# Kernel tuning notes

Measured on AMD Instinct MI355X. Metric: run time of the kernel, lower is better.

Reference implementation:

```python
import jax, jax.numpy as jnp
from jax import lax
import numpy as np

D, H, W3 = 240, 144, 240
V = D * H * W3  # 8294400 voxels


def conv3d(x, w, padding, stride=(1, 1, 1), b=None):
    y = lax.conv_general_dilated(x, w, window_strides=stride, padding=padding,
                                 dimension_numbers=('NCDHW', 'OIDHW', 'NCDHW'))
    if b is not None:
        y = y + b[None, :, None, None, None]
    return y


def downsample_block(x, w):
    # conv(c_in -> c_out - c_in, k3 s2 p1) concat maxpool(2,2), then relu
    c = conv3d(x, w, [(1, 1)] * 3, stride=(2, 2, 2))
    p = lax.reduce_window(x, -jnp.inf, lax.max, (1, 1, 2, 2, 2), (1, 1, 2, 2, 2), 'VALID')
    return jax.nn.relu(jnp.concatenate([c, p], axis=1))


def bottleneck(x, w_in, w133, b133, w331, b331, w313, b313, w_out):
    y0 = jax.nn.relu(conv3d(x, w_in, [(0, 0)] * 3))
    y1 = jax.nn.relu(conv3d(y0, w133, [(0, 0), (1, 1), (1, 1)], b=b133))
    y2 = jax.nn.relu(conv3d(y1, w331, [(1, 1), (1, 1), (0, 0)], b=b331) + y1)
    y3 = jax.nn.relu(conv3d(y2, w313, [(1, 1), (0, 0), (1, 1)], b=b313) + y2 + y1)
    return jax.nn.relu(conv3d(y3, w_out, [(0, 0)] * 3) + x)  # residual=True


def project2d_3d(feature2d, depth_3d):
    b, c, h, w = feature2d.shape
    flat = feature2d.reshape(b, c, h * w)

    def one(feat, depth):  # feat [c, HW], depth [HW]
        # pixels with depth<=0 are redirected out of bounds and dropped (stay zero)
        idx = jnp.where(depth > 0, depth, V)
        out = jnp.zeros((V, feat.shape[0]), feat.dtype).at[idx].set(feat.T, mode='drop')
        return out.T  # [c, V]

    return jax.vmap(one)(flat, depth_3d).reshape(b, c, D, H, W3)


def setup_inputs() -> dict:
    key = jax.random.key(0)
    ks = jax.random.split(key, 20)
    f = lambda i, shape: jax.random.normal(ks[i], shape, jnp.float32) * 0.05
    return {
        'feature2d': jax.random.normal(ks[0], (1, 12, 480, 640), jnp.float32),
        'depth_3d': jax.random.randint(ks[1], (1, 480 * 640), 0, V),
        'w_ds1': f(2, (4, 12, 3, 3, 3)),
        'b1_w_in': f(3, (4, 16, 1, 1, 1)),
        'b1_w133': f(4, (4, 4, 1, 3, 3)), 'b1_b133': f(5, (4,)),
        'b1_w331': f(6, (4, 4, 3, 3, 1)), 'b1_b331': f(7, (4,)),
        'b1_w313': f(8, (4, 4, 3, 1, 3)), 'b1_b313': f(9, (4,)),
        'b1_w_out': f(10, (16, 4, 1, 1, 1)),
        'w_ds2': f(11, (16, 16, 3, 3, 3)),
        'b2_w_in': f(12, (8, 32, 1, 1, 1)),
        'b2_w133': f(13, (8, 8, 1, 3, 3)), 'b2_b133': f(14, (8,)),
        'b2_w331': f(15, (8, 8, 3, 3, 1)), 'b2_b331': f(16, (8,)),
        'b2_w313': f(17, (8, 8, 3, 1, 3)), 'b2_b313': f(18, (8,)),
        'b2_w_out': f(19, (32, 8, 1, 1, 1)),
    }


def reference(feature2d, depth_3d, w_ds1,
              b1_w_in, b1_w133, b1_b133, b1_w331, b1_b331, b1_w313, b1_b313, b1_w_out,
              w_ds2,
              b2_w_in, b2_w133, b2_b133, b2_w331, b2_b331, b2_w313, b2_b313, b2_w_out):
    # location == 'late'
    segres = project2d_3d(feature2d, depth_3d)  # [b,12,240,144,240]
    # AvgPool3d(k=3, p=1, s=1) with count_include_pad=True -> window sum / 27
    pool = lax.reduce_window(segres, 0.0, lax.add, (1, 1, 3, 3, 3), (1, 1, 1, 1, 1),
                             [(0, 0), (0, 0), (1, 1), (1, 1), (1, 1)]) / 27.0
    segres = segres + pool * (segres == 0).astype(segres.dtype)
    x = downsample_block(segres, w_ds1)  # [b,16,120,72,120]
    x = bottleneck(x, b1_w_in, b1_w133, b1_b133, b1_w331, b1_b331, b1_w313, b1_b313, b1_w_out)
    x = downsample_block(x, w_ds2)  # [b,32,60,36,60]
    x = bottleneck(x, b2_w_in, b2_w133, b2_b133, b2_w331, b2_b331, b2_w313, b2_b313, b2_w_out)
    return x
```

## Files before the change

kernel.cpp:

```cpp
#include <hip/hip_runtime.h>
#include <hip/hip_bf16.h>

typedef __hip_bfloat16 bf16;
typedef unsigned short u16;

static __device__ __forceinline__ float lo16(unsigned u) { return __uint_as_float(u << 16); }
static __device__ __forceinline__ float hi16(unsigned u) { return __uint_as_float(u & 0xFFFF0000u); }
static __device__ __forceinline__ unsigned f2u(float x) {
    unsigned u = __float_as_uint(x);
    return (u + 0x7FFFu + ((u >> 16) & 1u)) >> 16;
}
static __device__ __forceinline__ unsigned pack2(float a, float b) {
    return f2u(a) | (f2u(b) << 16);
}

constexpr int D0 = 240, H0 = 144, W0 = 240;
constexpr int V  = D0 * H0 * W0;
constexpr int NPIX = 480 * 640;
constexpr int D1 = 120, H1 = 72, W1 = 120;
constexpr int N1 = D1 * H1 * W1;
constexpr int D2 = 60, H2 = 36, W2 = 60;
constexpr int N2 = D2 * H2 * W2;

constexpr size_t GRP_U16  = (size_t)V * 4;
constexpr size_t GRP_BYTES = GRP_U16 * sizeof(u16);
constexpr size_t SEG_BYTES = 3 * GRP_BYTES;
constexpr size_t WIN_BYTES = (size_t)V * sizeof(unsigned);
constexpr int ZCHUNKS  = (int)((SEG_BYTES + WIN_BYTES) / 16);
constexpr int WCHUNKS  = (int)(WIN_BYTES / 16);
constexpr size_t BIG_WS = SEG_BYTES + WIN_BYTES + GRP_BYTES;

__global__ void __launch_bounds__(256) kz_zero16(uint4* __restrict__ p, int nchunks) {
    int i = blockIdx.x * 256 + threadIdx.x;
    if (i >= nchunks) return;
    p[i] = make_uint4(0u, 0u, 0u, 0u);
}

__global__ void __launch_bounds__(256) kz_scatter_win(const int* __restrict__ depth,
                                                      unsigned* __restrict__ winner) {
    int p = blockIdx.x * 256 + threadIdx.x;
    if (p >= NPIX) return;
    int d = depth[p];
    if (d > 0 && d < V) atomicMax(&winner[d], (unsigned)(p + 1));
}

__global__ void __launch_bounds__(256) kz_scatter_write(const int* __restrict__ depth,
                                                        const unsigned* __restrict__ winner,
                                                        const float* __restrict__ feat,
                                                        u16* __restrict__ seg) {
    int p = blockIdx.x * 256 + threadIdx.x;
    if (p >= NPIX) return;
    int d = depth[p];
    if (d > 0 && d < V && winner[d] == (unsigned)(p + 1)) {
#pragma unroll
        for (int g = 0; g < 3; ++g) {
            uint2 val;
            val.x = pack2(feat[(4 * g + 0) * NPIX + p], feat[(4 * g + 1) * NPIX + p]);
            val.y = pack2(feat[(4 * g + 2) * NPIX + p], feat[(4 * g + 3) * NPIX + p]);
            *(uint2*)(seg + g * GRP_U16 + (size_t)d * 4) = val;
        }
    }
}

constexpr int FTW = 120;
constexpr int FROWS = 36;

template <bool GATED>
__global__ void __launch_bounds__(256) kz_fillL(const u16* __restrict__ rb,
                                                const unsigned* __restrict__ win,
                                                u16* __restrict__ fb) {
    __shared__ u16 S[FROWS * FTW * 4];
    int bid = blockIdx.x;
    int wt = bid & 1;
    int t1 = bid >> 1;
    int ht = t1 % 36;
    int dt = t1 / 36;
    int d0 = dt * 4, h0 = ht * 4, w0 = wt * 120;
    int tid = threadIdx.x;

    for (int tt = tid; tt < FROWS * 60; tt += 256) {
        int hr = tt / 60;
        int pt = tt - hr * 60;
        int w = w0 + 2 * pt;
        int d = d0 - 1 + hr / 6;
        int h = h0 - 1 + hr % 6;
        uint4 O = make_uint4(0u, 0u, 0u, 0u);
        if (d >= 0 && d < D0 && h >= 0 && h < H0) {
            size_t row = (size_t)(d * H0 + h) * W0;
            const u16* rp = rb + (row + w) * 4;
            uint4 X = *(const uint4*)(rp);
            if (GATED) {
                uint2 WN = *(const uint2*)(win + row + w);
                if (WN.x == 0u) { X.x = 0u; X.y = 0u; }
                if (WN.y == 0u) { X.z = 0u; X.w = 0u; }
            }
            float x0[4] = {lo16(X.x), hi16(X.x), lo16(X.y), hi16(X.y)};
            float x1[4] = {lo16(X.z), hi16(X.z), lo16(X.w), hi16(X.w)};
            float l[4] = {0.f, 0.f, 0.f, 0.f}, rr[4] = {0.f, 0.f, 0.f, 0.f};
            if (w > 0) {
                uint2 L = *(const uint2*)(rp - 4);
                if (GATED && win[row + w - 1] == 0u) { L.x = 0u; L.y = 0u; }
                l[0] = lo16(L.x); l[1] = hi16(L.x); l[2] = lo16(L.y); l[3] = hi16(L.y);
            }
            if (w < 238) {
                uint2 R = *(const uint2*)(rp + 8);
                if (GATED && win[row + w + 2] == 0u) { R.x = 0u; R.y = 0u; }
                rr[0] = lo16(R.x); rr[1] = hi16(R.x); rr[2] = lo16(R.y); rr[3] = hi16(R.y);
            }
            O.x = pack2(l[0] + x0[0] + x1[0], l[1] + x0[1] + x1[1]);
            O.y = pack2(l[2] + x0[2] + x1[2], l[3] + x0[3] + x1[3]);
            O.z = pack2(x0[0] + x1[0] + rr[0], x0[1] + x1[1] + rr[1]);
            O.w = pack2(x0[2] + x1[2] + rr[2], x0[3] + x1[3] + rr[3]);
        }
        *(uint4*)(S + ((size_t)hr * FTW + 2 * pt) * 4) = O;
    }
    __syncthreads();

    for (int ot = tid; ot < 16 * 60; ot += 256) {
        int orr = ot / 60;
        int pt = ot - orr * 60;
        int w = w0 + 2 * pt;
        int di = orr >> 2, hi_ = orr & 3;
        int d = d0 + di, h = h0 + hi_;
        float s[8] = {0.f, 0.f, 0.f, 0.f, 0.f, 0.f, 0.f, 0.f};
#pragma unroll
        for (int dd = 0; dd < 3; ++dd) {
#pragma unroll
            for (int dh = 0; dh < 3; ++dh) {
                int hr = (di + dd) * 6 + (hi_ + dh);
                uint4 T = *(const uint4*)(S + ((size_t)hr * FTW + 2 * pt) * 4);
                s[0] += lo16(T.x); s[1] += hi16(T.x); s[2] += lo16(T.y); s[3] += hi16(T.y);
                s[4] += lo16(T.z); s[5] += hi16(T.z); s[6] += lo16(T.w); s[7] += hi16(T.w);
            }
        }
        size_t row = (size_t)(d * H0 + h) * W0;
        size_t gi = (row + w) * 4;
        uint4 Rv = *(const uint4*)(rb + gi);
        if (GATED) {
            uint2 WN = *(const uint2*)(win + row + w);
            if (WN.x == 0u) { Rv.x = 0u; Rv.y = 0u; }
            if (WN.y == 0u) { Rv.z = 0u; Rv.w = 0u; }
        }
        constexpr float inv27 = 1.0f / 27.0f;
        uint4 Ov;
        Ov.x = ((Rv.x & 0x7FFFu) ? (Rv.x & 0xFFFFu) : f2u(s[0] * inv27))
             | ((((Rv.x >> 16) & 0x7FFFu) ? (Rv.x >> 16) : f2u(s[1] * inv27)) << 16);
        Ov.y = ((Rv.y & 0x7FFFu) ? (Rv.y & 0xFFFFu) : f2u(s[2] * inv27))
             | ((((Rv.y >> 16) & 0x7FFFu) ? (Rv.y >> 16) : f2u(s[3] * inv27)) << 16);
        Ov.z = ((Rv.z & 0x7FFFu) ? (Rv.z & 0xFFFFu) : f2u(s[4] * inv27))
             | ((((Rv.z >> 16) & 0x7FFFu) ? (Rv.z >> 16) : f2u(s[5] * inv27)) << 16);
        Ov.w = ((Rv.w & 0x7FFFu) ? (Rv.w & 0xFFFFu) : f2u(s[6] * inv27))
             | ((((Rv.w >> 16) & 0x7FFFu) ? (Rv.w >> 16) : f2u(s[7] * inv27)) << 16);
        *(uint4*)(fb + gi) = Ov;
    }
}

#define SEL2(ci, x0, x1) ((ci) == 0 ? lo16(x0) : (ci) == 1 ? hi16(x0) : (ci) == 2 ? lo16(x1) : hi16(x1))

template <bool FUSE_PW>
__global__ void __launch_bounds__(256) kz_ds1(const u16* __restrict__ f0g,
                                              const u16* __restrict__ f1g,
                                              const u16* __restrict__ f2g,
                                              const float* __restrict__ w,
                                              const float* __restrict__ wpw,
                                              float* __restrict__ x1i,
                                              float* __restrict__ y0o) {
    __shared__ float wl[12 * 27 * 4];
    __shared__ float wpl[64];
    for (int t = threadIdx.x; t < 12 * 27 * 4; t += 256) {
        int m = t & 3;
        int r = t >> 2;
        int tap = r % 27;
        int ci12 = r / 27;
        wl[t] = w[(m * 12 + ci12) * 27 + tap];
    }
    if (FUSE_PW && threadIdx.x < 64) wpl[threadIdx.x] = wpw[threadIdx.x];
    __syncthreads();
    int tq = blockIdx.x * 256 + threadIdx.x;
    if (tq >= N1 / 4) return;
    int q  = tq % 30;
    int t2 = tq / 30;
    int ho = t2 % H1;
    int d0 = t2 / H1;
    size_t o0 = (size_t)tq * 4;
    int vbase = 8 * q;

    const u16* bases[3] = {f0g, f1g, f2g};
    float acc[4][4];
    float mxp[3][4][4];
#pragma unroll
    for (int j = 0; j < 4; ++j)
#pragma unroll
        for (int m = 0; m < 4; ++m) acc[j][m] = 0.f;
#pragma unroll
    for (int g = 0; g < 3; ++g)
#pragma unroll
        for (int ci = 0; ci < 4; ++ci)
#pragma unroll
            for (int j = 0; j < 4; ++j) mxp[g][ci][j] = -1e30f;

#pragma unroll
    for (int g = 0; g < 3; ++g) {
        const u16* base = bases[g];
        const float* wg = wl + g * 432;
#pragma unroll 1
        for (int kd = 0; kd < 3; ++kd) {
            int d2 = 2 * d0 - 1 + kd;
            bool dv = (d2 >= 0 && d2 < D0);
#pragma unroll
            for (int kh = 0; kh < 3; ++kh) {
                int h2 = 2 * ho - 1 + kh;
                bool vv = dv && (h2 >= 0) && (h2 < H0);
                uint2 E = make_uint2(0u, 0u);
                uint4 A = make_uint4(0u, 0u, 0u, 0u);
                uint4 B = A, C = A, D = A;
                if (vv) {
                    const u16* rp = base + ((size_t)(d2 * H0 + h2) * W0 + vbase) * 4;
                    A = *(const uint4*)(rp);
                    B = *(const uint4*)(rp + 8);
                    C = *(const uint4*)(rp + 16);
                    D = *(const uint4*)(rp + 24);
                    if (q > 0) E = *(const uint2*)(rp - 4);
                }
                const float* wk = wg + (kd * 9 + kh * 3) * 4;
#pragma unroll
                for (int ci = 0; ci < 4; ++ci) {
                    float e  = SEL2(ci, E.x, E.y);
                    float a0 = SEL2(ci, A.x, A.y), a1 = SEL2(ci, A.z, A.w);
                    float b0 = SEL2(ci, B.x, B.y), b1 = SEL2(ci, B.z, B.w);
                    float c0 = SEL2(ci, C.x, C.y), c1 = SEL2(ci, C.z, C.w);
                    float e0 = SEL2(ci, D.x, D.y), e1 = SEL2(ci, D.z, D.w);
                    const float* wp_ = wk + ci * 108;
                    float4 wA = *(const float4*)(wp_);
                    float4 wB = *(const float4*)(wp_ + 4);
                    float4 wC = *(const float4*)(wp_ + 8);
                    acc[0][0] += e  * wA.x + a0 * wB.x + a1 * wC.x;
                    acc[0][1] += e  * wA.y + a0 * wB.y + a1 * wC.y;
                    acc[0][2] += e  * wA.z + a0 * wB.z + a1 * wC.z;
                    acc[0][3] += e  * wA.w + a0 * wB.w + a1 * wC.w;
                    acc[1][0] += a1 * wA.x + b0 * wB.x + b1 * wC.x;
                    acc[1][1] += a1 * wA.y + b0 * wB.y + b1 * wC.y;
                    acc[1][2] += a1 * wA.z + b0 * wB.z + b1 * wC.z;
                    acc[1][3] += a1 * wA.w + b0 * wB.w + b1 * wC.w;
                    acc[2][0] += b1 * wA.x + c0 * wB.x + c1 * wC.x;
                    acc[2][1] += b1 * wA.y + c0 * wB.y + c1 * wC.y;
                    acc[2][2] += b1 * wA.z + c0 * wB.z + c1 * wC.z;
                    acc[2][3] += b1 * wA.w + c0 * wB.w + c1 * wC.w;
                    acc[3][0] += c1 * wA.x + e0 * wB.x + e1 * wC.x;
                    acc[3][1] += c1 * wA.y + e0 * wB.y + e1 * wC.y;
                    acc[3][2] += c1 * wA.z + e0 * wB.z + e1 * wC.z;
                    acc[3][3] += c1 * wA.w + e0 * wB.w + e1 * wC.w;
                    if (kh >= 1 && kd >= 1) {
                        mxp[g][ci][0] = fmaxf(mxp[g][ci][0], fmaxf(a0, a1));
                        mxp[g][ci][1] = fmaxf(mxp[g][ci][1], fmaxf(b0, b1));
                        mxp[g][ci][2] = fmaxf(mxp[g][ci][2], fmaxf(c0, c1));
                        mxp[g][ci][3] = fmaxf(mxp[g][ci][3], fmaxf(e0, e1));
                    }
                }
            }
        }
    }
#pragma unroll
    for (int j = 0; j < 4; ++j) {
        float x1v[16];
        x1v[0] = fmaxf(acc[j][0], 0.f); x1v[1] = fmaxf(acc[j][1], 0.f);
        x1v[2] = fmaxf(acc[j][2], 0.f); x1v[3] = fmaxf(acc[j][3], 0.f);
#pragma unroll
        for (int g = 0; g < 3; ++g) {
            x1v[4 + 4 * g + 0] = fmaxf(mxp[g][0][j], 0.f);
            x1v[4 + 4 * g + 1] = fmaxf(mxp[g][1][j], 0.f);
            x1v[4 + 4 * g + 2] = fmaxf(mxp[g][2][j], 0.f);
            x1v[4 + 4 * g + 3] = fmaxf(mxp[g][3][j], 0.f);
        }
        float* xo = x1i + (o0 + j) * 16;
        *(float4*)(xo)      = make_float4(x1v[0], x1v[1], x1v[2], x1v[3]);
        *(float4*)(xo + 4)  = make_float4(x1v[4], x1v[5], x1v[6], x1v[7]);
        *(float4*)(xo + 8)  = make_float4(x1v[8], x1v[9], x1v[10], x1v[11]);
        *(float4*)(xo + 12) = make_float4(x1v[12], x1v[13], x1v[14], x1v[15]);
        if (FUSE_PW) {
            float y[4];
#pragma unroll
            for (int m = 0; m < 4; ++m) {
                const float* wm = wpl + m * 16;
                float r = 0.f;
#pragma unroll
                for (int k = 0; k < 16; ++k) r += x1v[k] * wm[k];
                y[m] = fmaxf(r, 0.f);
            }
            *(float4*)(y0o + (o0 + j) * 4) = make_float4(y[0], y[1], y[2], y[3]);
        }
    }
}

__global__ void __launch_bounds__(256) kz_pw16to4i(const float* __restrict__ in,
                                                   const float* __restrict__ w,
                                                   float* __restrict__ out) {
    __shared__ float wl[64];
    if (threadIdx.x < 64) wl[threadIdx.x] = w[threadIdx.x];
    __syncthreads();
    int o = blockIdx.x * 256 + threadIdx.x;
    const float* ip = in + (size_t)o * 16;
    float4 A = *(const float4*)(ip);
    float4 B = *(const float4*)(ip + 4);
    float4 C = *(const float4*)(ip + 8);
    float4 D = *(const float4*)(ip + 12);
    float r[4];
#pragma unroll
    for (int m = 0; m < 4; ++m) {
        const float* wm = wl + m * 16;
        r[m] = A.x * wm[0] + A.y * wm[1] + A.z * wm[2] + A.w * wm[3]
             + B.x * wm[4] + B.y * wm[5] + B.z * wm[6] + B.w * wm[7]
             + C.x * wm[8] + C.y * wm[9] + C.z * wm[10] + C.w * wm[11]
             + D.x * wm[12] + D.y * wm[13] + D.z * wm[14] + D.w * wm[15];
    }
    *(float4*)(out + (size_t)o * 4) = make_float4(fmaxf(r[0], 0.f), fmaxf(r[1], 0.f),
                                                  fmaxf(r[2], 0.f), fmaxf(r[3], 0.f));
}

template <int KD, int KH, int KW, int NADD>
__global__ void __launch_bounds__(256) kz_bconv4i(const float* __restrict__ in,
                                                  const float* __restrict__ w,
                                                  const float* __restrict__ b,
                                                  const float* __restrict__ add1,
                                                  const float* __restrict__ add2,
                                                  float* __restrict__ out) {
    constexpr int S = KD * KH * KW;
    __shared__ float wl[16 * S];
    __shared__ float bl[4];
    for (int t = threadIdx.x; t < 16 * S; t += 256) {
        int m = t & 3;
        int r = t >> 2;
        int ci = r & 3;
        int tap = r >> 2;
        wl[t] = w[(m * 4 + ci) * S + tap];
    }
    if (threadIdx.x < 4) bl[threadIdx.x] = b[threadIdx.x];
    __syncthreads();
    int o = blockIdx.x * 256 + threadIdx.x;
    int wo = o % W1;
    int t  = o / W1;
    int ho = t % H1;
    int d0 = t / H1;
    float a0 = bl[0], a1 = bl[1], a2 = bl[2], a3 = bl[3];
#pragma unroll
    for (int kd = 0; kd < KD; ++kd) {
        int d2 = d0 + kd - KD / 2;
        if (KD > 1 && (d2 < 0 || d2 >= D1)) continue;
#pragma unroll
        for (int kh = 0; kh < KH; ++kh) {
            int h2 = ho + kh - KH / 2;
            if (KH > 1 && (h2 < 0 || h2 >= H1)) continue;
#pragma unroll
            for (int kw = 0; kw < KW; ++kw) {
                int w2 = wo + kw - KW / 2;
                if (KW > 1 && (w2 < 0 || w2 >= W1)) continue;
                float4 v = *(const float4*)(in + (size_t)((d2 * H1 + h2) * W1 + w2) * 4);
                int tap = (kd * KH + kh) * KW + kw;
                const float* wt = wl + tap * 16;
                float4 w0 = *(const float4*)(wt);
                float4 w1 = *(const float4*)(wt + 4);
                float4 w2v = *(const float4*)(wt + 8);
                float4 w3 = *(const float4*)(wt + 12);
                a0 += v.x * w0.x + v.y * w1.x + v.z * w2v.x + v.w * w3.x;
                a1 += v.x * w0.y + v.y * w1.y + v.z * w2v.y + v.w * w3.y;
                a2 += v.x * w0.z + v.y * w1.z + v.z * w2v.z + v.w * w3.z;
                a3 += v.x * w0.w + v.y * w1.w + v.z * w2v.w + v.w * w3.w;
            }
        }
    }
    if (NADD >= 1) {
        float4 r1 = *(const float4*)(add1 + (size_t)o * 4);
        a0 += r1.x; a1 += r1.y; a2 += r1.z; a3 += r1.w;
    }
    if (NADD >= 2) {
        float4 r2 = *(const float4*)(add2 + (size_t)o * 4);
        a0 += r2.x; a1 += r2.y; a2 += r2.z; a3 += r2.w;
    }
    *(float4*)(out + (size_t)o * 4) = make_float4(fmaxf(a0, 0.f), fmaxf(a1, 0.f),
                                                  fmaxf(a2, 0.f), fmaxf(a3, 0.f));
}

__global__ void __launch_bounds__(256) kz_bconv4i_pw(const float* __restrict__ in,
                                                     const float* __restrict__ w,
                                                     const float* __restrict__ b,
                                                     const float* __restrict__ add1,
                                                     const float* __restrict__ add2,
                                                     const float* __restrict__ wp,
                                                     const float* __restrict__ x1i,
                                                     float* __restrict__ out) {
    constexpr int S = 9;
    __shared__ float wl[16 * S];
    __shared__ float bl[4];
    __shared__ float wpl[64];
    for (int t = threadIdx.x; t < 16 * S; t += 256) {
        int m = t & 3;
        int r = t >> 2;
        int ci = r & 3;
        int tap = r >> 2;
        wl[t] = w[(m * 4 + ci) * S + tap];
    }
    if (threadIdx.x < 4) bl[threadIdx.x] = b[threadIdx.x];
    if (threadIdx.x < 64) wpl[threadIdx.x] = wp[threadIdx.x];
    __syncthreads();
    int o = blockIdx.x * 256 + threadIdx.x;
    int wo = o % W1;
    int t  = o / W1;
    int ho = t % H1;
    int d0 = t / H1;
    float a0 = bl[0], a1 = bl[1], a2 = bl[2], a3 = bl[3];
#pragma unroll
    for (int kd = 0; kd < 3; ++kd) {
        int d2 = d0 + kd - 1;
        if (d2 < 0 || d2 >= D1) continue;
#pragma unroll
        for (int kw = 0; kw < 3; ++kw) {
            int w2 = wo + kw - 1;
            if (w2 < 0 || w2 >= W1) continue;
            float4 v = *(const float4*)(in + (size_t)((d2 * H1 + ho) * W1 + w2) * 4);
            int tap = kd * 3 + kw;
            const float* wt = wl + tap * 16;
            float4 w0 = *(const float4*)(wt);
            float4 w1 = *(const float4*)(wt + 4);
            float4 w2v = *(const float4*)(wt + 8);
            float4 w3 = *(const float4*)(wt + 12);
            a0 += v.x * w0.x + v.y * w1.x + v.z * w2v.x + v.w * w3.x;
            a1 += v.x * w0.y + v.y * w1.y + v.z * w2v.y + v.w * w3.y;
            a2 += v.x * w0.z + v.y * w1.z + v.z * w2v.z + v.w * w3.z;
            a3 += v.x * w0.w + v.y * w1.w + v.z * w2v.w + v.w * w3.w;
        }
    }
    float4 r1 = *(const float4*)(add1 + (size_t)o * 4);
    float4 r2 = *(const float4*)(add2 + (size_t)o * 4);
    float y0 = fmaxf(a0 + r1.x + r2.x, 0.f);
    float y1 = fmaxf(a1 + r1.y + r2.y, 0.f);
    float y2 = fmaxf(a2 + r1.z + r2.z, 0.f);
    float y3 = fmaxf(a3 + r1.w + r2.w, 0.f);
    const float* rp = x1i + (size_t)o * 16;
    float4 R0 = *(const float4*)(rp);
    float4 R1 = *(const float4*)(rp + 4);
    float4 R2 = *(const float4*)(rp + 8);
    float4 R3 = *(const float4*)(rp + 12);
    float rr[16] = {R0.x, R0.y, R0.z, R0.w, R1.x, R1.y, R1.z, R1.w,
                    R2.x, R2.y, R2.z, R2.w, R3.x, R3.y, R3.z, R3.w};
#pragma unroll
    for (int m = 0; m < 16; ++m) {
        const float* wm = wpl + m * 4;
        float r = y0 * wm[0] + y1 * wm[1] + y2 * wm[2] + y3 * wm[3] + rr[m];
        out[(size_t)m * N1 + o] = fmaxf(r, 0.f);
    }
}

__global__ void __launch_bounds__(256) kz_ds2f(const float* __restrict__ in,
                                               const float* __restrict__ w,
                                               const float* __restrict__ wz,
                                               float* __restrict__ out,
                                               float* __restrict__ z0i) {
    __shared__ float wl[16 * 27 * 16];
    __shared__ float wzl[256];
    for (int t = threadIdx.x; t < 16 * 27 * 16; t += 256) {
        int m = t & 15;
        int r = t >> 4;
        int tap = r % 27;
        int ci = r / 27;
        wl[t] = w[(m * 16 + ci) * 27 + tap];
    }
    if (threadIdx.x < 256) {
        int m = threadIdx.x & 7;
        int k = threadIdx.x >> 3;
        wzl[threadIdx.x] = wz[m * 32 + k];
    }
    __syncthreads();
    int o = blockIdx.x * 256 + threadIdx.x;
    if (o >= N2) return;
    int wo = o % W2;
    int t  = o / W2;
    int ho = t % H2;
    int d0 = t / H2;
    float acc[16];
    float zacc[8];
#pragma unroll
    for (int m = 0; m < 16; ++m) acc[m] = 0.f;
#pragma unroll
    for (int m = 0; m < 8; ++m) zacc[m] = 0.f;
#pragma unroll 1
    for (int ci = 0; ci < 16; ++ci) {
        const float* base = in + ci * N1;
        const float* wci = wl + ci * 432;
        float mx = -1e30f;
#pragma unroll 1
        for (int kd = 0; kd < 3; ++kd) {
            int d2 = 2 * d0 - 1 + kd;
            bool dv = (d2 >= 0 && d2 < D1);
#pragma unroll
            for (int kh = 0; kh < 3; ++kh) {
                int h2 = 2 * ho - 1 + kh;
                bool rvv = dv && (h2 >= 0 && h2 < H1);
                float vm1 = 0.f, v0 = 0.f, v1 = 0.f;
                if (rvv) {
                    int r2 = (d2 * H1 + h2) * W1 + 2 * wo;
                    float2 pb = *(const float2*)(base + r2);
                    v0 = pb.x; v1 = pb.y;
                    if (wo > 0) {
                        float2 pa = *(const float2*)(base + r2 - 2);
                        vm1 = pa.y;
                    }
                }
                const float* wk = wci + (kd * 9 + kh * 3) * 16;
#pragma unroll
                for (int q = 0; q < 4; ++q) {
                    float4 wA = *(const float4*)(wk + q * 4);
                    float4 wB = *(const float4*)(wk + 16 + q * 4);
                    float4 wC = *(const float4*)(wk + 32 + q * 4);
                    acc[4 * q + 0] += vm1 * wA.x + v0 * wB.x + v1 * wC.x;
                    acc[4 * q + 1] += vm1 * wA.y + v0 * wB.y + v1 * wC.y;
                    acc[4 * q + 2] += vm1 * wA.z + v0 * wB.z + v1 * wC.z;
                    acc[4 * q + 3] += vm1 * wA.w + v0 * wB.w + v1 * wC.w;
                }
                if (kd >= 1 && kh >= 1) mx = fmaxf(mx, fmaxf(v0, v1));
            }
        }
        float pl = fmaxf(mx, 0.f);
        out[(16 + ci) * N2 + o] = pl;
        {
            const float* wq = wzl + (16 + ci) * 8;
            float4 z0 = *(const float4*)(wq);
            float4 z1 = *(const float4*)(wq + 4);
            zacc[0] += z0.x * pl; zacc[1] += z0.y * pl; zacc[2] += z0.z * pl; zacc[3] += z0.w * pl;
            zacc[4] += z1.x * pl; zacc[5] += z1.y * pl; zacc[6] += z1.z * pl; zacc[7] += z1.w * pl;
        }
    }
#pragma unroll
    for (int j = 0; j < 16; ++j) {
        float cj = fmaxf(acc[j], 0.f);
        out[j * N2 + o] = cj;
        const float* wq = wzl + j * 8;
        float4 z0 = *(const float4*)(wq);
        float4 z1 = *(const float4*)(wq + 4);
        zacc[0] += z0.x * cj; zacc[1] += z0.y * cj; zacc[2] += z0.z * cj; zacc[3] += z0.w * cj;
        zacc[4] += z1.x * cj; zacc[5] += z1.y * cj; zacc[6] += z1.z * cj; zacc[7] += z1.w * cj;
    }
    float* op = z0i + (size_t)o * 8;
    *(float4*)(op)     = make_float4(fmaxf(zacc[0], 0.f), fmaxf(zacc[1], 0.f),
                                     fmaxf(zacc[2], 0.f), fmaxf(zacc[3], 0.f));
    *(float4*)(op + 4) = make_float4(fmaxf(zacc[4], 0.f), fmaxf(zacc[5], 0.f),
                                     fmaxf(zacc[6], 0.f), fmaxf(zacc[7], 0.f));
}

template <int KD, int KH, int KW, int NADD>
__global__ void __launch_bounds__(256) kz_bconv8i(const float* __restrict__ in,
                                                  const float* __restrict__ w,
                                                  const float* __restrict__ b,
                                                  const float* __restrict__ add1,
                                                  const float* __restrict__ add2,
                                                  float* __restrict__ out) {
    constexpr int S = KD * KH * KW;
    __shared__ float wl[64 * S];
    __shared__ float bl[8];
    for (int t = threadIdx.x; t < 64 * S; t += 256) {
        int m = t & 7;
        int r = t >> 3;
        int ci = r & 7;
        int tap = r >> 3;
        wl[t] = w[(m * 8 + ci) * S + tap];
    }
    if (threadIdx.x < 8) bl[threadIdx.x] = b[threadIdx.x];
    __syncthreads();
    int o = blockIdx.x * 256 + threadIdx.x;
    if (o >= N2) return;
    int wo = o % W2;
    int t  = o / W2;
    int ho = t % H2;
    int d0 = t / H2;
    float acc[8];
#pragma unroll
    for (int m = 0; m < 8; ++m) acc[m] = bl[m];
#pragma unroll
    for (int kd = 0; kd < KD; ++kd) {
        int d2 = d0 + kd - KD / 2;
        if (KD > 1 && (d2 < 0 || d2 >= D2)) continue;
#pragma unroll
        for (int kh = 0; kh < KH; ++kh) {
            int h2 = ho + kh - KH / 2;
            if (KH > 1 && (h2 < 0 || h2 >= H2)) continue;
#pragma unroll
            for (int kw = 0; kw < KW; ++kw) {
                int w2 = wo + kw - KW / 2;
                if (KW > 1 && (w2 < 0 || w2 >= W2)) continue;
                const float* vp = in + (size_t)((d2 * H2 + h2) * W2 + w2) * 8;
                float4 v0 = *(const float4*)(vp);
                float4 v1 = *(const float4*)(vp + 4);
                float vv[8] = {v0.x, v0.y, v0.z, v0.w, v1.x, v1.y, v1.z, v1.w};
                int tap = (kd * KH + kh) * KW + kw;
                const float* wt = wl + tap * 64;
#pragma unroll
                for (int ci = 0; ci < 8; ++ci) {
                    float vc = vv[ci];
                    float4 wa = *(const float4*)(wt + ci * 8);
                    float4 wb = *(const float4*)(wt + ci * 8 + 4);
                    acc[0] += vc * wa.x; acc[1] += vc * wa.y;
                    acc[2] += vc * wa.z; acc[3] += vc * wa.w;
                    acc[4] += vc * wb.x; acc[5] += vc * wb.y;
                    acc[6] += vc * wb.z; acc[7] += vc * wb.w;
                }
            }
        }
    }
    if (NADD >= 1) {
        const float* ap = add1 + (size_t)o * 8;
        float4 r0 = *(const float4*)(ap), r1 = *(const float4*)(ap + 4);
        acc[0] += r0.x; acc[1] += r0.y; acc[2] += r0.z; acc[3] += r0.w;
        acc[4] += r1.x; acc[5] += r1.y; acc[6] += r1.z; acc[7] += r1.w;
    }
    if (NADD >= 2) {
        const float* ap = add2 + (size_t)o * 8;
        float4 r0 = *(const float4*)(ap), r1 = *(const float4*)(ap + 4);
        acc[0] += r0.x; acc[1] += r0.y; acc[2] += r0.z; acc[3] += r0.w;
        acc[4] += r1.x; acc[5] += r1.y; acc[6] += r1.z; acc[7] += r1.w;
    }
    float* op = out + (size_t)o * 8;
    *(float4*)(op)     = make_float4(fmaxf(acc[0], 0.f), fmaxf(acc[1], 0.f),
                                     fmaxf(acc[2], 0.f), fmaxf(acc[3], 0.f));
    *(float4*)(op + 4) = make_float4(fmaxf(acc[4], 0.f), fmaxf(acc[5], 0.f),
                                     fmaxf(acc[6], 0.f), fmaxf(acc[7], 0.f));
}

__global__ void __launch_bounds__(256) kz_bconv8i_pw(const float* __restrict__ in,
                                                     const float* __restrict__ w,
                                                     const float* __restrict__ b,
                                                     const float* __restrict__ add1,
                                                     const float* __restrict__ add2,
                                                     const float* __restrict__ wp,
                                                     const float* __restrict__ resp,
                                                     float* __restrict__ out) {
    constexpr int S = 9;
    __shared__ float wl[64 * S];
    __shared__ float bl[8];
    __shared__ float wpl[256];
    for (int t = threadIdx.x; t < 64 * S; t += 256) {
        int m = t & 7;
        int r = t >> 3;
        int ci = r & 7;
        int tap = r >> 3;
        wl[t] = w[(m * 8 + ci) * S + tap];
    }
    if (threadIdx.x < 8) bl[threadIdx.x] = b[threadIdx.x];
    if (threadIdx.x < 256) wpl[threadIdx.x] = wp[threadIdx.x];
    __syncthreads();
    int o = blockIdx.x * 256 + threadIdx.x;
    if (o >= N2) return;
    int wo = o % W2;
    int t  = o / W2;
    int ho = t % H2;
    int d0 = t / H2;
    float acc[8];
#pragma unroll
    for (int m = 0; m < 8; ++m) acc[m] = bl[m];
#pragma unroll
    for (int kd = 0; kd < 3; ++kd) {
        int d2 = d0 + kd - 1;
        if (d2 < 0 || d2 >= D2) continue;
#pragma unroll
        for (int kw = 0; kw < 3; ++kw) {
            int w2 = wo + kw - 1;
            if (w2 < 0 || w2 >= W2) continue;
            const float* vp = in + (size_t)((d2 * H2 + ho) * W2 + w2) * 8;
            float4 v0 = *(const float4*)(vp);
            float4 v1 = *(const float4*)(vp + 4);
            float vv[8] = {v0.x, v0.y, v0.z, v0.w, v1.x, v1.y, v1.z, v1.w};
            int tap = kd * 3 + kw;
            const float* wt = wl + tap * 64;
#pragma unroll
            for (int ci = 0; ci < 8; ++ci) {
                float vc = vv[ci];
                float4 wa = *(const float4*)(wt + ci * 8);
                float4 wb = *(const float4*)(wt + ci * 8 + 4);
                acc[0] += vc * wa.x; acc[1] += vc * wa.y;
                acc[2] += vc * wa.z; acc[3] += vc * wa.w;
                acc[4] += vc * wb.x; acc[5] += vc * wb.y;
                acc[6] += vc * wb.z; acc[7] += vc * wb.w;
            }
        }
    }
    {
        const float* ap = add1 + (size_t)o * 8;
        float4 r0 = *(const float4*)(ap), r1 = *(const float4*)(ap + 4);
        acc[0] += r0.x; acc[1] += r0.y; acc[2] += r0.z; acc[3] += r0.w;
        acc[4] += r1.x; acc[5] += r1.y; acc[6] += r1.z; acc[7] += r1.w;
    }
    {
        const float* ap = add2 + (size_t)o * 8;
        float4 r0 = *(const float4*)(ap), r1 = *(const float4*)(ap + 4);
        acc[0] += r0.x; acc[1] += r0.y; acc[2] += r0.z; acc[3] += r0.w;
        acc[4] += r1.x; acc[5] += r1.y; acc[6] += r1.z; acc[7] += r1.w;
    }
#pragma unroll
    for (int m = 0; m < 8; ++m) acc[m] = fmaxf(acc[m], 0.f);
#pragma unroll
    for (int m = 0; m < 32; ++m) {
        const float* wm = wpl + m * 8;
        float r = acc[0] * wm[0] + acc[1] * wm[1] + acc[2] * wm[2] + acc[3] * wm[3]
                + acc[4] * wm[4] + acc[5] * wm[5] + acc[6] * wm[6] + acc[7] * wm[7];
        r += resp[(size_t)m * N2 + o];
        out[(size_t)m * N2 + o] = fmaxf(r, 0.f);
    }
}

extern "C" void kernel_launch(void* const* d_in, const int* in_sizes, int n_in,
                              void* d_out, int out_size, void* d_ws, size_t ws_size,
                              hipStream_t stream) {
    const float* feat   = (const float*)d_in[0];
    const int*   depth  = (const int*)d_in[1];
    const float* w_ds1  = (const float*)d_in[2];
    const float* b1_win = (const float*)d_in[3];
    const float* b1w133 = (const float*)d_in[4];
    const float* b1b133 = (const float*)d_in[5];
    const float* b1w331 = (const float*)d_in[6];
    const float* b1b331 = (const float*)d_in[7];
    const float* b1w313 = (const float*)d_in[8];
    const float* b1b313 = (const float*)d_in[9];
    const float* b1wout = (const float*)d_in[10];
    const float* w_ds2  = (const float*)d_in[11];
    const float* b2_win = (const float*)d_in[12];
    const float* b2w133 = (const float*)d_in[13];
    const float* b2b133 = (const float*)d_in[14];
    const float* b2w331 = (const float*)d_in[15];
    const float* b2b331 = (const float*)d_in[16];
    const float* b2w313 = (const float*)d_in[17];
    const float* b2b313 = (const float*)d_in[18];
    const float* b2wout = (const float*)d_in[19];

    char* base = (char*)d_ws;
    const bool bigws = (ws_size >= BIG_WS);

    u16* raw0 = (u16*)base;
    u16* raw1 = (u16*)(base + GRP_BYTES);
    u16* raw2 = (u16*)(base + 2 * GRP_BYTES);
    unsigned* winner = (unsigned*)(base + SEG_BYTES);
    u16* fil0 = bigws ? (u16*)(base + SEG_BYTES + WIN_BYTES) : (u16*)(base + SEG_BYTES);
    u16* fil1 = (u16*)base;
    u16* fil2 = (u16*)(base + GRP_BYTES);
    float* x1i = (float*)(base + 2 * GRP_BYTES);
    float* y0i = bigws ? (float*)(base + SEG_BYTES) : (float*)base;
    float* y1i = bigws ? (float*)base : (float*)base + 4 * N1;
    float* y2i = y1i + 4 * N1;
    float* x1b = (float*)(base + SEG_BYTES);
    float* x2  = (float*)base;
    float* z0i = x2 + 32 * N2;
    float* z1i = z0i + 8 * N2;
    float* z2i = z1i + 8 * N2;

    float* out = (float*)d_out;

    if (bigws) {
        kz_zero16<<<WCHUNKS / 256, 256, 0, stream>>>((uint4*)winner, WCHUNKS);
    } else {
        kz_zero16<<<ZCHUNKS / 256, 256, 0, stream>>>((uint4*)base, ZCHUNKS);
    }

    kz_scatter_win  <<<NPIX / 256, 256, 0, stream>>>(depth, winner);
    kz_scatter_write<<<NPIX / 256, 256, 0, stream>>>(depth, winner, feat, raw0);

    if (bigws) {
        kz_fillL<true><<<4320, 256, 0, stream>>>(raw0, winner, fil0);
        kz_fillL<true><<<4320, 256, 0, stream>>>(raw1, winner, fil1);
        kz_fillL<true><<<4320, 256, 0, stream>>>(raw2, winner, fil2);
    } else {
        kz_fillL<false><<<4320, 256, 0, stream>>>(raw0, nullptr, fil0);
        kz_fillL<false><<<4320, 256, 0, stream>>>(raw1, nullptr, fil1);
        kz_fillL<false><<<4320, 256, 0, stream>>>(raw2, nullptr, fil2);
    }

    if (bigws) {
        kz_ds1<true><<<(N1 / 4 + 255) / 256, 256, 0, stream>>>(fil0, fil1, fil2, w_ds1,
                                                               b1_win, x1i, y0i);
    } else {
        kz_ds1<false><<<(N1 / 4 + 255) / 256, 256, 0, stream>>>(fil0, fil1, fil2, w_ds1,
                                                                nullptr, x1i, nullptr);
        kz_pw16to4i<<<N1 / 256, 256, 0, stream>>>(x1i, b1_win, y0i);
    }

    kz_bconv4i<1, 3, 3, 0><<<N1 / 256, 256, 0, stream>>>(y0i, b1w133, b1b133, nullptr, nullptr, y1i);
    kz_bconv4i<3, 3, 1, 1><<<N1 / 256, 256, 0, stream>>>(y1i, b1w331, b1b331, y1i, nullptr, y2i);
    kz_bconv4i_pw<<<N1 / 256, 256, 0, stream>>>(y2i, b1w313, b1b313, y2i, y1i, b1wout, x1i, x1b);

    kz_ds2f<<<(N2 + 255) / 256, 256, 0, stream>>>(x1b, w_ds2, b2_win, x2, z0i);

    kz_bconv8i<1, 3, 3, 0><<<(N2 + 255) / 256, 256, 0, stream>>>(z0i, b2w133, b2b133, nullptr, nullptr, z1i);
    kz_bconv8i<3, 3, 1, 1><<<(N2 + 255) / 256, 256, 0, stream>>>(z1i, b2w331, b2b331, z1i, nullptr, z2i);
    kz_bconv8i_pw<<<(N2 + 255) / 256, 256, 0, stream>>>(z2i, b2w313, b2b313, z2i, z1i, b2wout, x2, out);

    (void)in_sizes; (void)n_in; (void)out_size;
}
```

Measured before the change: 649.0 us.

## Register-block bottleneck convs and ds2 over consecutive W outputs

The stage-1 bottleneck conv kernels now have each thread compute four consecutive W outputs, loading a six-voxel row strip once and reusing it across the three kw taps. The final pointwise step writes float4 vectors. The stage-2 downsample kernel computes two adjacent outputs per thread, sharing overlapping input loads and writing float2. This cuts redundant global loads and index arithmetic, at the cost of more registers per thread and fewer threads in flight.

```diff
diff --git a/kernel.cpp b/kernel.cpp
--- a/kernel.cpp
+++ b/kernel.cpp
@@ -318,7 +318,7 @@
 }
 
 template <int KD, int KH, int KW, int NADD>
-__global__ void __launch_bounds__(256) kz_bconv4i(const float* __restrict__ in,
+__global__ void __launch_bounds__(256) kz_bconv4p(const float* __restrict__ in,
                                                   const float* __restrict__ w,
                                                   const float* __restrict__ b,
                                                   const float* __restrict__ add1,
@@ -336,12 +336,18 @@
     }
     if (threadIdx.x < 4) bl[threadIdx.x] = b[threadIdx.x];
     __syncthreads();
-    int o = blockIdx.x * 256 + threadIdx.x;
-    int wo = o % W1;
-    int t  = o / W1;
-    int ho = t % H1;
-    int d0 = t / H1;
-    float a0 = bl[0], a1 = bl[1], a2 = bl[2], a3 = bl[3];
+    int tq = blockIdx.x * 256 + threadIdx.x;
+    if (tq >= N1 / 4) return;
+    int q  = tq % 30;
+    int t2 = tq / 30;
+    int ho = t2 % H1;
+    int d0 = t2 / H1;
+    size_t o0 = (size_t)tq * 4;
+    float acc[4][4];
+#pragma unroll
+    for (int j = 0; j < 4; ++j) {
+        acc[j][0] = bl[0]; acc[j][1] = bl[1]; acc[j][2] = bl[2]; acc[j][3] = bl[3];
+    }
 #pragma unroll
     for (int kd = 0; kd < KD; ++kd) {
         int d2 = d0 + kd - KD / 2;
@@ -350,37 +356,78 @@
         for (int kh = 0; kh < KH; ++kh) {
             int h2 = ho + kh - KH / 2;
             if (KH > 1 && (h2 < 0 || h2 >= H1)) continue;
-#pragma unroll
-            for (int kw = 0; kw < KW; ++kw) {
-                int w2 = wo + kw - KW / 2;
-                if (KW > 1 && (w2 < 0 || w2 >= W1)) continue;
-                float4 v = *(const float4*)(in + (size_t)((d2 * H1 + h2) * W1 + w2) * 4);
-                int tap = (kd * KH + kh) * KW + kw;
+            const float* rowp = in + (size_t)((d2 * H1 + h2) * W1 + 4 * q) * 4;
+            if (KW == 3) {
+                float4 vv[6];
+                vv[1] = *(const float4*)(rowp);
+                vv[2] = *(const float4*)(rowp + 4);
+                vv[3] = *(const float4*)(rowp + 8);
+                vv[4] = *(const float4*)(rowp + 12);
+                vv[0] = (q > 0)  ? *(const float4*)(rowp - 4)  : make_float4(0.f, 0.f, 0.f, 0.f);
+                vv[5] = (q < 29) ? *(const float4*)(rowp + 16) : make_float4(0.f, 0.f, 0.f, 0.f);
+#pragma unroll
+                for (int kw = 0; kw < 3; ++kw) {
+                    int tap = (kd * KH + kh) * 3 + kw;
+                    const float* wt = wl + tap * 16;
+                    float4 w0 = *(const float4*)(wt);
+                    float4 w1 = *(const float4*)(wt + 4);
+                    float4 w2v = *(const float4*)(wt + 8);
+                    float4 w3 = *(const float4*)(wt + 12);
+#pragma unroll
+                    for (int j = 0; j < 4; ++j) {
+                        float4 v = vv[j + kw];
+                        acc[j][0] += v.x * w0.x + v.y * w1.x + v.z * w2v.x + v.w * w3.x;
+                        acc[j][1] += v.x * w0.y + v.y * w1.y + v.z * w2v.y + v.w * w3.y;
+                        acc[j][2] += v.x * w0.z + v.y * w1.z + v.z * w2v.z + v.w * w3.z;
+                        acc[j][3] += v.x * w0.w + v.y * w1.w + v.z * w2v.w + v.w * w3.w;
+                    }
+                }
+            } else {
+                float4 vv[4];
+                vv[0] = *(const float4*)(rowp);
+                vv[1] = *(const float4*)(rowp + 4);
+                vv[2] = *(const float4*)(rowp + 8);
+                vv[3] = *(const float4*)(rowp + 12);
+                int tap = kd * KH + kh;
                 const float* wt = wl + tap * 16;
                 float4 w0 = *(const float4*)(wt);
                 float4 w1 = *(const float4*)(wt + 4);
                 float4 w2v = *(const float4*)(wt + 8);
                 float4 w3 = *(const float4*)(wt + 12);
-                a0 += v.x * w0.x + v.y * w1.x + v.z * w2v.x + v.w * w3.x;
-                a1 += v.x * w0.y + v.y * w1.y + v.z * w2v.y + v.w * w3.y;
-                a2 += v.x * w0.z + v.y * w1.z + v.z * w2v.z + v.w * w3.z;
-                a3 += v.x * w0.w + v.y * w1.w + v.z * w2v.w + v.w * w3.w;
+#pragma unroll
+                for (int j = 0; j < 4; ++j) {
+                    float4 v = vv[j];
+                    acc[j][0] += v.x * w0.x + v.y * w1.x + v.z * w2v.x + v.w * w3.x;
+                    acc[j][1] += v.x * w0.y + v.y * w1.y + v.z * w2v.y + v.w * w3.y;
+                    acc[j][2] += v.x * w0.z + v.y * w1.z + v.z * w2v.z + v.w * w3.z;
+                    acc[j][3] += v.x * w0.w + v.y * w1.w + v.z * w2v.w + v.w * w3.w;
+                }
             }
         }
     }
     if (NADD >= 1) {
-        float4 r1 = *(const float4*)(add1 + (size_t)o * 4);
-        a0 += r1.x; a1 += r1.y; a2 += r1.z; a3 += r1.w;
+#pragma unroll
+        for (int j = 0; j < 4; ++j) {
+            float4 r1 = *(const float4*)(add1 + (o0 + j) * 4);
+            acc[j][0] += r1.x; acc[j][1] += r1.y; acc[j][2] += r1.z; acc[j][3] += r1.w;
+        }
     }
     if (NADD >= 2) {
-        float4 r2 = *(const float4*)(add2 + (size_t)o * 4);
-        a0 += r2.x; a1 += r2.y; a2 += r2.z; a3 += r2.w;
-    }
-    *(float4*)(out + (size_t)o * 4) = make_float4(fmaxf(a0, 0.f), fmaxf(a1, 0.f),
-                                                  fmaxf(a2, 0.f), fmaxf(a3, 0.f));
-}
-
-__global__ void __launch_bounds__(256) kz_bconv4i_pw(const float* __restrict__ in,
+#pragma unroll
+        for (int j = 0; j < 4; ++j) {
+            float4 r2 = *(const float4*)(add2 + (o0 + j) * 4);
+            acc[j][0] += r2.x; acc[j][1] += r2.y; acc[j][2] += r2.z; acc[j][3] += r2.w;
+        }
+    }
+#pragma unroll
+    for (int j = 0; j < 4; ++j) {
+        *(float4*)(out + (o0 + j) * 4) =
+            make_float4(fmaxf(acc[j][0], 0.f), fmaxf(acc[j][1], 0.f),
+                        fmaxf(acc[j][2], 0.f), fmaxf(acc[j][3], 0.f));
+    }
+}
+
+__global__ void __launch_bounds__(256) kz_bconv4p_pw(const float* __restrict__ in,
                                                      const float* __restrict__ w,
                                                      const float* __restrict__ b,
                                                      const float* __restrict__ add1,
@@ -402,59 +449,88 @@
     if (threadIdx.x < 4) bl[threadIdx.x] = b[threadIdx.x];
     if (threadIdx.x < 64) wpl[threadIdx.x] = wp[threadIdx.x];
     __syncthreads();
-    int o = blockIdx.x * 256 + threadIdx.x;
-    int wo = o % W1;
-    int t  = o / W1;
-    int ho = t % H1;
-    int d0 = t / H1;
-    float a0 = bl[0], a1 = bl[1], a2 = bl[2], a3 = bl[3];
+    int tq = blockIdx.x * 256 + threadIdx.x;
+    if (tq >= N1 / 4) return;
+    int q  = tq % 30;
+    int t2 = tq / 30;
+    int ho = t2 % H1;
+    int d0 = t2 / H1;
+    size_t o0 = (size_t)tq * 4;
+    float acc[4][4];
+#pragma unroll
+    for (int j = 0; j < 4; ++j) {
+        acc[j][0] = bl[0]; acc[j][1] = bl[1]; acc[j][2] = bl[2]; acc[j][3] = bl[3];
+    }
 #pragma unroll
     for (int kd = 0; kd < 3; ++kd) {
         int d2 = d0 + kd - 1;
         if (d2 < 0 || d2 >= D1) continue;
+        const float* rowp = in + (size_t)((d2 * H1 + ho) * W1 + 4 * q) * 4;
+        float4 vv[6];
+        vv[1] = *(const float4*)(rowp);
+        vv[2] = *(const float4*)(rowp + 4);
+        vv[3] = *(const float4*)(rowp + 8);
+        vv[4] = *(const float4*)(rowp + 12);
+        vv[0] = (q > 0)  ? *(const float4*)(rowp - 4)  : make_float4(0.f, 0.f, 0.f, 0.f);
+        vv[5] = (q < 29) ? *(const float4*)(rowp + 16) : make_float4(0.f, 0.f, 0.f, 0.f);
 #pragma unroll
         for (int kw = 0; kw < 3; ++kw) {
-            int w2 = wo + kw - 1;
-            if (w2 < 0 || w2 >= W1) continue;
-            float4 v = *(const float4*)(in + (size_t)((d2 * H1 + ho) * W1 + w2) * 4);
             int tap = kd * 3 + kw;
             const float* wt = wl + tap * 16;
             float4 w0 = *(const float4*)(wt);
             float4 w1 = *(const float4*)(wt + 4);
             float4 w2v = *(const float4*)(wt + 8);
             float4 w3 = *(const float4*)(wt + 12);
-            a0 += v.x * w0.x + v.y * w1.x + v.z * w2v.x + v.w * w3.x;
-            a1 += v.x * w0.y + v.y * w1.y + v.z * w2v.y + v.w * w3.y;
-            a2 += v.x * w0.z + v.y * w1.z + v.z * w2v.z + v.w * w3.z;
-            a3 += v.x * w0.w + v.y * w1.w + v.z * w2v.w + v.w * w3.w;
-        }
-    }
-    float4 r1 = *(const float4*)(add1 + (size_t)o * 4);
-    float4 r2 = *(const float4*)(add2 + (size_t)o * 4);
-    float y0 = fmaxf(a0 + r1.x + r2.x, 0.f);
-    float y1 = fmaxf(a1 + r1.y + r2.y, 0.f);
-    float y2 = fmaxf(a2 + r1.z + r2.z, 0.f);
-    float y3 = fmaxf(a3 + r1.w + r2.w, 0.f);
-    const float* rp = x1i + (size_t)o * 16;
-    float4 R0 = *(const float4*)(rp);
-    float4 R1 = *(const float4*)(rp + 4);
-    float4 R2 = *(const float4*)(rp + 8);
-    float4 R3 = *(const float4*)(rp + 12);
-    float rr[16] = {R0.x, R0.y, R0.z, R0.w, R1.x, R1.y, R1.z, R1.w,
-                    R2.x, R2.y, R2.z, R2.w, R3.x, R3.y, R3.z, R3.w};
+#pragma unroll
+            for (int j = 0; j < 4; ++j) {
+                float4 v = vv[j + kw];
+                acc[j][0] += v.x * w0.x + v.y * w1.x + v.z * w2v.x + v.w * w3.x;
+                acc[j][1] += v.x * w0.y + v.y * w1.y + v.z * w2v.y + v.w * w3.y;
+                acc[j][2] += v.x * w0.z + v.y * w1.z + v.z * w2v.z + v.w * w3.z;
+                acc[j][3] += v.x * w0.w + v.y * w1.w + v.z * w2v.w + v.w * w3.w;
+            }
+        }
+    }
+    float y[4][4];
+#pragma unroll
+    for (int j = 0; j < 4; ++j) {
+        float4 r1 = *(const float4*)(add1 + (o0 + j) * 4);
+        float4 r2 = *(const float4*)(add2 + (o0 + j) * 4);
+        y[j][0] = fmaxf(acc[j][0] + r1.x + r2.x, 0.f);
+        y[j][1] = fmaxf(acc[j][1] + r1.y + r2.y, 0.f);
+        y[j][2] = fmaxf(acc[j][2] + r1.z + r2.z, 0.f);
+        y[j][3] = fmaxf(acc[j][3] + r1.w + r2.w, 0.f);
+    }
+    float rr[4][16];
+#pragma unroll
+    for (int j = 0; j < 4; ++j) {
+        const float* rp = x1i + (o0 + j) * 16;
+        float4 R0 = *(const float4*)(rp);
+        float4 R1 = *(const float4*)(rp + 4);
+        float4 R2 = *(const float4*)(rp + 8);
+        float4 R3 = *(const float4*)(rp + 12);
+        rr[j][0] = R0.x; rr[j][1] = R0.y; rr[j][2] = R0.z; rr[j][3] = R0.w;
+        rr[j][4] = R1.x; rr[j][5] = R1.y; rr[j][6] = R1.z; rr[j][7] = R1.w;
+        rr[j][8] = R2.x; rr[j][9] = R2.y; rr[j][10] = R2.z; rr[j][11] = R2.w;
+        rr[j][12] = R3.x; rr[j][13] = R3.y; rr[j][14] = R3.z; rr[j][15] = R3.w;
+    }
 #pragma unroll
     for (int m = 0; m < 16; ++m) {
         const float* wm = wpl + m * 4;
-        float r = y0 * wm[0] + y1 * wm[1] + y2 * wm[2] + y3 * wm[3] + rr[m];
-        out[(size_t)m * N1 + o] = fmaxf(r, 0.f);
-    }
-}
-
-__global__ void __launch_bounds__(256) kz_ds2f(const float* __restrict__ in,
-                                               const float* __restrict__ w,
-                                               const float* __restrict__ wz,
-                                               float* __restrict__ out,
-                                               float* __restrict__ z0i) {
+        float4 ov;
+        ov.x = fmaxf(y[0][0] * wm[0] + y[0][1] * wm[1] + y[0][2] * wm[2] + y[0][3] * wm[3] + rr[0][m], 0.f);
+        ov.y = fmaxf(y[1][0] * wm[0] + y[1][1] * wm[1] + y[1][2] * wm[2] + y[1][3] * wm[3] + rr[1][m], 0.f);
+        ov.z = fmaxf(y[2][0] * wm[0] + y[2][1] * wm[1] + y[2][2] * wm[2] + y[2][3] * wm[3] + rr[2][m], 0.f);
+        ov.w = fmaxf(y[3][0] * wm[0] + y[3][1] * wm[1] + y[3][2] * wm[2] + y[3][3] * wm[3] + rr[3][m], 0.f);
+        *(float4*)(out + (size_t)m * N1 + o0) = ov;
+    }
+}
+
+__global__ void __launch_bounds__(256) kz_ds2fp(const float* __restrict__ in,
+                                                const float* __restrict__ w,
+                                                const float* __restrict__ wz,
+                                                float* __restrict__ out,
+                                                float* __restrict__ z0i) {
     __shared__ float wl[16 * 27 * 16];
     __shared__ float wzl[256];
     for (int t = threadIdx.x; t < 16 * 27 * 16; t += 256) {
@@ -470,23 +546,27 @@
         wzl[threadIdx.x] = wz[m * 32 + k];
     }
     __syncthreads();
-    int o = blockIdx.x * 256 + threadIdx.x;
-    if (o >= N2) return;
-    int wo = o % W2;
-    int t  = o / W2;
-    int ho = t % H2;
-    int d0 = t / H2;
-    float acc[16];
-    float zacc[8];
-#pragma unroll
-    for (int m = 0; m < 16; ++m) acc[m] = 0.f;
-#pragma unroll
-    for (int m = 0; m < 8; ++m) zacc[m] = 0.f;
+    int tp = blockIdx.x * 256 + threadIdx.x;
+    if (tp >= N2 / 2) return;
+    int q  = tp % 30;
+    int t2 = tp / 30;
+    int ho = t2 % H2;
+    int d0 = t2 / H2;
+    size_t o0 = (size_t)tp * 2;
+    float acc[2][16];
+    float zacc[2][8];
+#pragma unroll
+    for (int j = 0; j < 2; ++j) {
+#pragma unroll
+        for (int m = 0; m < 16; ++m) acc[j][m] = 0.f;
+#pragma unroll
+        for (int m = 0; m < 8; ++m) zacc[j][m] = 0.f;
+    }
 #pragma unroll 1
     for (int ci = 0; ci < 16; ++ci) {
         const float* base = in + ci * N1;
         const float* wci = wl + ci * 432;
-        float mx = -1e30f;
+        float mx0 = -1e30f, mx1 = -1e30f;
 #pragma unroll 1
         for (int kd = 0; kd < 3; ++kd) {
             int d2 = 2 * d0 - 1 + kd;
@@ -495,55 +575,70 @@
             for (int kh = 0; kh < 3; ++kh) {
                 int h2 = 2 * ho - 1 + kh;
                 bool rvv = dv && (h2 >= 0 && h2 < H1);
-                float vm1 = 0.f, v0 = 0.f, v1 = 0.f;
+                float vin[5] = {0.f, 0.f, 0.f, 0.f, 0.f};
                 if (rvv) {
-                    int r2 = (d2 * H1 + h2) * W1 + 2 * wo;
-                    float2 pb = *(const float2*)(base + r2);
-                    v0 = pb.x; v1 = pb.y;
-                    if (wo > 0) {
+                    int r2 = (d2 * H1 + h2) * W1 + 4 * q;
+                    float4 pb = *(const float4*)(base + r2);
+                    vin[1] = pb.x; vin[2] = pb.y; vin[3] = pb.z; vin[4] = pb.w;
+                    if (q > 0) {
                         float2 pa = *(const float2*)(base + r2 - 2);
-                        vm1 = pa.y;
+                        vin[0] = pa.y;
                     }
                 }
                 const float* wk = wci + (kd * 9 + kh * 3) * 16;
 #pragma unroll
-                for (int q = 0; q < 4; ++q) {
-                    float4 wA = *(const float4*)(wk + q * 4);
-                    float4 wB = *(const float4*)(wk + 16 + q * 4);
-                    float4 wC = *(const float4*)(wk + 32 + q * 4);
-                    acc[4 * q + 0] += vm1 * wA.x + v0 * wB.x + v1 * wC.x;
-                    acc[4 * q + 1] += vm1 * wA.y + v0 * wB.y + v1 * wC.y;
-                    acc[4 * q + 2] += vm1 * wA.z + v0 * wB.z + v1 * wC.z;
-                    acc[4 * q + 3] += vm1 * wA.w + v0 * wB.w + v1 * wC.w;
+                for (int q4 = 0; q4 < 4; ++q4) {
+                    float4 wA = *(const float4*)(wk + q4 * 4);
+                    float4 wB = *(const float4*)(wk + 16 + q4 * 4);
+                    float4 wC = *(const float4*)(wk + 32 + q4 * 4);
+                    acc[0][4 * q4 + 0] += vin[0] * wA.x + vin[1] * wB.x + vin[2] * wC.x;
+                    acc[0][4 * q4 + 1] += vin[0] * wA.y + vin[1] * wB.y + vin[2] * wC.y;
+                    acc[0][4 * q4 + 2] += vin[0] * wA.z + vin[1] * wB.z + vin[2] * wC.z;
+                    acc[0][4 * q4 + 3] += vin[0] * wA.w + vin[1] * wB.w + vin[2] * wC.w;
+                    acc[1][4 * q4 + 0] += vin[2] * wA.x + vin[3] * wB.x + vin[4] * wC.x;
+                    acc[1][4 * q4 + 1] += vin[2] * wA.y + vin[3] * wB.y + vin[4] * wC.y;
+                    acc[1][4 * q4 + 2] += vin[2] * wA.z + vin[3] * wB.z + vin[4] * wC.z;
+                    acc[1][4 * q4 + 3] += vin[2] * wA.w + vin[3] * wB.w + vin[4] * wC.w;
                 }
-                if (kd >= 1 && kh >= 1) mx = fmaxf(mx, fmaxf(v0, v1));
-            }
-        }
-        float pl = fmaxf(mx, 0.f);
-        out[(16 + ci) * N2 + o] = pl;
+                if (kd >= 1 && kh >= 1) {
+                    mx0 = fmaxf(mx0, fmaxf(vin[1], vin[2]));
+                    mx1 = fmaxf(mx1, fmaxf(vin[3], vin[4]));
+                }
+            }
+        }
+        float pl0 = fmaxf(mx0, 0.f), pl1 = fmaxf(mx1, 0.f);
+        *(float2*)(out + (size_t)(16 + ci) * N2 + o0) = make_float2(pl0, pl1);
         {
             const float* wq = wzl + (16 + ci) * 8;
             float4 z0 = *(const float4*)(wq);
             float4 z1 = *(const float4*)(wq + 4);
-            zacc[0] += z0.x * pl; zacc[1] += z0.y * pl; zacc[2] += z0.z * pl; zacc[3] += z0.w * pl;
-            zacc[4] += z1.x * pl; zacc[5] += z1.y * pl; zacc[6] += z1.z * pl; zacc[7] += z1.w * pl;
-        }
-    }
-#pragma unroll
-    for (int j = 0; j < 16; ++j) {
-        float cj = fmaxf(acc[j], 0.f);
-        out[j * N2 + o] = cj;
-        const float* wq = wzl + j * 8;
+            zacc[0][0] += z0.x * pl0; zacc[0][1] += z0.y * pl0; zacc[0][2] += z0.z * pl0; zacc[0][3] += z0.w * pl0;
+            zacc[0][4] += z1.x * pl0; zacc[0][5] += z1.y * pl0; zacc[0][6] += z1.z * pl0; zacc[0][7] += z1.w * pl0;
+            zacc[1][0] += z0.x * pl1; zacc[1][1] += z0.y * pl1; zacc[1][2] += z0.z * pl1; zacc[1][3] += z0.w * pl1;
+            zacc[1][4] += z1.x * pl1; zacc[1][5] += z1.y * pl1; zacc[1][6] += z1.z * pl1; zacc[1][7] += z1.w * pl1;
+        }
+    }
+#pragma unroll
+    for (int jc = 0; jc < 16; ++jc) {
+        float c0 = fmaxf(acc[0][jc], 0.f);
+        float c1 = fmaxf(acc[1][jc], 0.f);
+        *(float2*)(out + (size_t)jc * N2 + o0) = make_float2(c0, c1);
+        const float* wq = wzl + jc * 8;
         float4 z0 = *(const float4*)(wq);
         float4 z1 = *(const float4*)(wq + 4);
-        zacc[0] += z0.x * cj; zacc[1] += z0.y * cj; zacc[2] += z0.z * cj; zacc[3] += z0.w * cj;
-        zacc[4] += z1.x * cj; zacc[5] += z1.y * cj; zacc[6] += z1.z * cj; zacc[7] += z1.w * cj;
-    }
-    float* op = z0i + (size_t)o * 8;
-    *(float4*)(op)     = make_float4(fmaxf(zacc[0], 0.f), fmaxf(zacc[1], 0.f),
-                                     fmaxf(zacc[2], 0.f), fmaxf(zacc[3], 0.f));
-    *(float4*)(op + 4) = make_float4(fmaxf(zacc[4], 0.f), fmaxf(zacc[5], 0.f),
-                                     fmaxf(zacc[6], 0.f), fmaxf(zacc[7], 0.f));
+        zacc[0][0] += z0.x * c0; zacc[0][1] += z0.y * c0; zacc[0][2] += z0.z * c0; zacc[0][3] += z0.w * c0;
+        zacc[0][4] += z1.x * c0; zacc[0][5] += z1.y * c0; zacc[0][6] += z1.z * c0; zacc[0][7] += z1.w * c0;
+        zacc[1][0] += z0.x * c1; zacc[1][1] += z0.y * c1; zacc[1][2] += z0.z * c1; zacc[1][3] += z0.w * c1;
+        zacc[1][4] += z1.x * c1; zacc[1][5] += z1.y * c1; zacc[1][6] += z1.z * c1; zacc[1][7] += z1.w * c1;
+    }
+#pragma unroll
+    for (int j = 0; j < 2; ++j) {
+        float* op = z0i + (o0 + j) * 8;
+        *(float4*)(op)     = make_float4(fmaxf(zacc[j][0], 0.f), fmaxf(zacc[j][1], 0.f),
+                                         fmaxf(zacc[j][2], 0.f), fmaxf(zacc[j][3], 0.f));
+        *(float4*)(op + 4) = make_float4(fmaxf(zacc[j][4], 0.f), fmaxf(zacc[j][5], 0.f),
+                                         fmaxf(zacc[j][6], 0.f), fmaxf(zacc[j][7], 0.f));
+    }
 }
 
 template <int KD, int KH, int KW, int NADD>
@@ -779,11 +874,11 @@
         kz_pw16to4i<<<N1 / 256, 256, 0, stream>>>(x1i, b1_win, y0i);
     }
 
-    kz_bconv4i<1, 3, 3, 0><<<N1 / 256, 256, 0, stream>>>(y0i, b1w133, b1b133, nullptr, nullptr, y1i);
-    kz_bconv4i<3, 3, 1, 1><<<N1 / 256, 256, 0, stream>>>(y1i, b1w331, b1b331, y1i, nullptr, y2i);
-    kz_bconv4i_pw<<<N1 / 256, 256, 0, stream>>>(y2i, b1w313, b1b313, y2i, y1i, b1wout, x1i, x1b);
-
-    kz_ds2f<<<(N2 + 255) / 256, 256, 0, stream>>>(x1b, w_ds2, b2_win, x2, z0i);
+    kz_bconv4p<1, 3, 3, 0><<<(N1 / 4 + 255) / 256, 256, 0, stream>>>(y0i, b1w133, b1b133, nullptr, nullptr, y1i);
+    kz_bconv4p<3, 3, 1, 1><<<(N1 / 4 + 255) / 256, 256, 0, stream>>>(y1i, b1w331, b1b331, y1i, nullptr, y2i);
+    kz_bconv4p_pw<<<(N1 / 4 + 255) / 256, 256, 0, stream>>>(y2i, b1w313, b1b313, y2i, y1i, b1wout, x1i, x1b);
+
+    kz_ds2fp<<<(N2 / 2 + 255) / 256, 256, 0, stream>>>(x1b, w_ds2, b2_win, x2, z0i);
 
     kz_bconv8i<1, 3, 3, 0><<<(N2 + 255) / 256, 256, 0, stream>>>(z0i, b2w133, b2b133, nullptr, nullptr, z1i);
     kz_bconv8i<3, 3, 1, 1><<<(N2 + 255) / 256, 256, 0, stream>>>(z1i, b2w331, b2b331, z1i, nullptr, z2i);
```

After: 718.0 us. 1.11x slower.
